# Optimization experiments

Measured on AMD Instinct MI355X. Metric: run time of the kernel, lower is better.

Reference implementation:

```python
import jax, jax.numpy as jnp
import numpy as np

B, CIN, MID, OUT = 4096, 64, 256, 256
K = CIN * 25  # flattened 5x5 patch per channel
EPS = 1e-5


def _masks():
    # [3, 25] binary masks over the 5x5 kernel for the 3 branch families
    circle = np.zeros((5, 5), np.float32); circle[1:4, 1:4] = 1.0
    corner = np.zeros((5, 5), np.float32)
    for (i, j) in [(0, 0), (0, 4), (4, 0), (4, 4), (2, 2)]:
        corner[i, j] = 1.0
    horse = np.zeros((5, 5), np.float32)
    for (i, j) in [(0, 1), (0, 3), (1, 0), (1, 4), (3, 0), (3, 4), (4, 1), (4, 3), (2, 2)]:
        horse[i, j] = 1.0
    return jnp.asarray(np.stack([circle, corner, horse]).reshape(3, 25))


def mish(x):
    return x * jnp.tanh(jax.nn.softplus(x))


def setup_inputs() -> dict:
    key = jax.random.key(0)
    ks = jax.random.split(key, 12)
    x = jax.random.normal(ks[0], (B, CIN, 7, 7), jnp.float32)
    W5 = jax.random.normal(ks[1], (27, MID, K), jnp.float32) * 0.05
    b5 = jax.random.normal(ks[2], (27, MID), jnp.float32) * 0.05
    gamma = jnp.ones((27, MID), jnp.float32)
    beta = jnp.zeros((27, MID), jnp.float32)
    run_mean = jax.random.normal(ks[3], (27, MID), jnp.float32) * 0.05
    run_var = jax.random.uniform(ks[4], (27, MID), jnp.float32, 0.5, 1.5)
    W1 = jax.random.normal(ks[5], (27, MID, MID), jnp.float32) * 0.05
    b1 = jax.random.normal(ks[6], (27, MID), jnp.float32) * 0.05
    W2 = jax.random.normal(ks[7], (27, OUT, MID), jnp.float32) * 0.05
    b2 = jax.random.normal(ks[8], (27, OUT), jnp.float32) * 0.05
    return {"x": x, "W5": W5, "b5": b5, "gamma": gamma, "beta": beta,
            "run_mean": run_mean, "run_var": run_var,
            "W1": W1, "b1": b1, "W2": W2, "b2": b2}


def reference(x, W5, b5, gamma, beta, run_mean, run_var, W1, b1, W2, b2):
    masks = _masks()  # [3,25]
    # 9 patches of 5x5: [9, B, CIN*25]
    patches = jnp.stack([x[:, :, k:k + 5, v:v + 5]
                         for k in range(3) for v in range(3)])
    patches = patches.reshape(9, B, K)
    # mask kernels per branch family and group weights as [3,9,MID,K]
    mask_k = jnp.repeat(masks, 9, axis=0)          # [27,25]
    mask_k = jnp.tile(mask_k, (1, CIN))[:, None, :]  # [27,1,CIN*25]
    W5m = (W5 * mask_k).reshape(3, 9, MID, K)
    # masked 5x5 conv on 5x5 patch -> 1x1 == dot product: [3,9,B,MID]
    z = jnp.einsum('pbk,gpmk->gpbm', patches, W5m) + b5.reshape(3, 9, 1, MID)
    # BatchNorm (inference, running stats) + Mish
    inv = jax.lax.rsqrt(run_var.reshape(3, 9, 1, MID) + EPS)
    h = mish((z - run_mean.reshape(3, 9, 1, MID)) * inv
             * gamma.reshape(3, 9, 1, MID) + beta.reshape(3, 9, 1, MID))
    # 1x1 conv + Mish, then final 1x1 conv
    h = mish(jnp.einsum('gpbm,gpnm->gpbn', h, W1.reshape(3, 9, MID, MID))
             + b1.reshape(3, 9, 1, MID))
    o = jnp.einsum('gpbm,gpom->gpbo', h, W2.reshape(3, 9, OUT, MID)) \
        + b2.reshape(3, 9, 1, OUT)                 # [3,9,B,OUT]
    copy_features = o[0].sum(0)                    # sum of 9 circle branches
    jump_features = o[1].sum(0) + o[2].sum(0)      # sum of 18 corner+horse
    # output is 1x1 spatially, so flatten(2).sum(2) is identity on [B,OUT]
    return copy_features * jump_features
```

## Files before the change

### kernel.cpp

```cpp
#include <hip/hip_runtime.h>

typedef __bf16 bf16x8 __attribute__((ext_vector_type(8)));
typedef float f32x4 __attribute__((ext_vector_type(4)));

__constant__ int SL_I[3][9] = {{1,1,1,2,2,2,3,3,3},{0,0,2,4,4,0,0,0,0},{0,0,1,1,2,3,3,4,4}};
__constant__ int SL_J[3][9] = {{1,2,3,1,2,3,1,2,3},{0,4,2,0,4,0,0,0,0},{1,3,0,4,2,0,4,1,3}};
__constant__ int SL_S[3][9] = {{6,7,8,11,12,13,16,17,18},{0,4,12,20,24,0,0,0,0},{1,3,5,9,12,15,19,21,23}};

#define GLDS16(gsrc, ldst)                                                        \
  __builtin_amdgcn_global_load_lds(                                               \
      (const __attribute__((address_space(1))) unsigned int*)(gsrc),              \
      (__attribute__((address_space(3))) unsigned int*)(ldst), 16, 0, 0)

static __device__ __forceinline__ unsigned short f2b(float f) {
  return __builtin_bit_cast(unsigned short, (__bf16)f);
}
static __device__ __forceinline__ float b2f(unsigned short u) {
  unsigned int b = ((unsigned int)u) << 16;
  return __builtin_bit_cast(float, b);
}
static __device__ __forceinline__ float mish_f(float x) {
  float u = __expf(x);
  float w = u * (u + 2.0f);
  float r = x * w * __builtin_amdgcn_rcpf(w + 2.0f);
  return (x > 20.0f) ? x : r;
}
static __device__ __forceinline__ int swz8(int c, int r) {
  return ((((c >> 3) ^ (r & 7)) << 3) | (c & 7));
}
static __device__ __forceinline__ int swoff(int c, int r) {
  return (c & ~63) | ((c & 63) ^ ((r & 7) << 3));
}

__global__ __launch_bounds__(256) void prep_x_k(const float* __restrict__ X,
                                                unsigned short* __restrict__ Xb) {
  __shared__ float tile[3136];
  const int b = blockIdx.x;
  const float* xp = X + (size_t)b * 3136;
  for (int i = threadIdx.x; i < 3136; i += 256) tile[i] = xp[i];
  __syncthreads();
  for (int i = threadIdx.x; i < 3136; i += 256) {
    int s = i >> 6, c = i & 63;
    Xb[(size_t)s * 262144 + (size_t)b * 64 + swz8(c, b)] = f2b(tile[c * 49 + s]);
  }
}

__global__ __launch_bounds__(256) void prep_w5_k(const float* __restrict__ W5,
                                                 unsigned short* __restrict__ W5c) {
  int idx = blockIdx.x * 256 + threadIdx.x;
  if (idx >= 27 * 256 * 9 * 64) return;
  int c = idx & 63;
  int t2 = idx >> 6;
  int u = t2 % 9;
  int gm = t2 / 9;
  int m = gm & 255;
  int g = (gm >> 8) / 9;
  int nm = (g == 1) ? 5 : 9;
  if (u >= nm) return;
  int c_src = swz8(c, m);
  W5c[idx] = f2b(W5[(size_t)gm * 1600 + c_src * 25 + SL_S[g][u]]);
}

__global__ __launch_bounds__(256) void prep_w12_k(const float* __restrict__ W1, const float* __restrict__ W2,
                                                  unsigned short* __restrict__ W1b, unsigned short* __restrict__ W2b) {
  int idx = blockIdx.x * 256 + threadIdx.x;
  if (idx < 27 * 256 * 256) {
    int n = (idx >> 8) & 255;
    int c = idx & 63;
    int src = (idx & ~63) | swz8(c, n);
    W1b[idx] = f2b(W1[src]);
    W2b[idx] = f2b(W2[src]);
  }
}

__global__ __launch_bounds__(256) void prep_bn_k(const float* __restrict__ b5, const float* __restrict__ gamma,
                                                 const float* __restrict__ beta, const float* __restrict__ rmean,
                                                 const float* __restrict__ rvar,
                                                 float* __restrict__ bn_a, float* __restrict__ bn_c) {
  int i = blockIdx.x * 256 + threadIdx.x;
  if (i < 27 * 256) {
    float a = gamma[i] * rsqrtf(rvar[i] + 1e-5f);
    bn_a[i] = a;
    bn_c[i] = (b5[i] - rmean[i]) * a + beta[i];
  }
}

__global__ __launch_bounds__(512) void gemm1_k(const unsigned short* __restrict__ Xb,
                                               const unsigned short* __restrict__ W5c,
                                               const float* __restrict__ bn_a, const float* __restrict__ bn_c,
                                               unsigned short* __restrict__ H) {
  __shared__ unsigned short smem[32768];
  const int t = threadIdx.x;
  const int lane = t & 63;
  const int w = t >> 6;
  const int wm = w >> 2, wn = w & 3;
  const int l15 = lane & 15, l4 = lane >> 4;
  const int sw = l15 & 7;
  const int m0 = blockIdx.x * 128, n0 = blockIdx.y * 128;
  const int gp = blockIdx.z;
  const int g = gp / 9, p = gp - g * 9;
  const int pk = p / 3, pv = p - pk * 3;
  const int nm = (g == 1) ? 5 : 9;

  const f32x4 zero = {0.f, 0.f, 0.f, 0.f};
  f32x4 acc[4][2];
#pragma unroll
  for (int i = 0; i < 4; ++i)
#pragma unroll
    for (int j = 0; j < 2; ++j) acc[i][j] = zero;

  auto STAGE = [&](int pbuf, int u) {
    const int s = (pk + SL_I[g][u]) * 7 + (pv + SL_J[g][u]);
    const unsigned short* srcA = Xb + (size_t)s * 262144 + (size_t)m0 * 64;
    unsigned short* dA = smem + pbuf * 16384;
    unsigned short* dB = dA + 8192;
#pragma unroll
    for (int it = 0; it < 2; ++it) {
      int idx = it * 512 + t;
      GLDS16(srcA + idx * 8, dA + idx * 8);
    }
#pragma unroll
    for (int it = 0; it < 2; ++it) {
      int idx = it * 512 + t;
      int row = idx >> 3, ch = idx & 7;
      GLDS16(W5c + (size_t)(gp * 256 + n0 + row) * 576 + u * 64 + ch * 8, dB + idx * 8);
    }
  };

  STAGE(0, 0);
  __syncthreads();
  int cur = 0;
  for (int u = 0; u < nm; ++u) {
    if (u + 1 < nm) STAGE(cur ^ 1, u + 1);
    const unsigned short* lA = smem + cur * 16384;
    const unsigned short* lB = lA + 8192;
#pragma unroll
    for (int kk = 0; kk < 2; ++kk) {
      bf16x8 af[4], bfr[2];
#pragma unroll
      for (int f4 = 0; f4 < 4; ++f4)
        af[f4] = *reinterpret_cast<const bf16x8*>(lA + (wm * 64 + f4 * 16 + l15) * 64 + (((kk * 4 + l4) ^ sw) << 3));
#pragma unroll
      for (int f2 = 0; f2 < 2; ++f2)
        bfr[f2] = *reinterpret_cast<const bf16x8*>(lB + (wn * 32 + f2 * 16 + l15) * 64 + (((kk * 4 + l4) ^ sw) << 3));
#pragma unroll
      for (int i = 0; i < 4; ++i)
#pragma unroll
        for (int j = 0; j < 2; ++j)
          acc[i][j] = __builtin_amdgcn_mfma_f32_16x16x32_bf16(af[i], bfr[j], acc[i][j], 0, 0, 0);
    }
    __syncthreads();
    cur ^= 1;
  }
#pragma unroll
  for (int j = 0; j < 2; ++j) {
    const int col = wn * 32 + j * 16 + l15;
    const float a  = bn_a[gp * 256 + n0 + col];
    const float cc = bn_c[gp * 256 + n0 + col];
#pragma unroll
    for (int i = 0; i < 4; ++i) {
      const int r0 = wm * 64 + i * 16 + l4 * 4;
#pragma unroll
      for (int e = 0; e < 4; ++e) {
        const int r = r0 + e;
        float z = acc[i][j][e] * a + cc;
        smem[r * 128 + (col ^ ((r & 7) << 3))] = f2b(mish_f(z));
      }
    }
  }
  __syncthreads();
  {
    unsigned short* Hg = H + (size_t)gp * 1048576;
#pragma unroll
    for (int it = 0; it < 4; ++it) {
      int idx = it * 512 + t;
      int row = idx >> 4, seg = idx & 15;
      int c8 = (seg * 8) ^ ((row & 7) << 3);
      uint4 v = *(const uint4*)(smem + row * 128 + c8);
      int colout = n0 + (seg >> 3) * 64 + (((seg & 7) ^ (row & 7)) << 3);
      *(uint4*)(Hg + (size_t)(m0 + row) * 256 + colout) = v;
    }
  }
}

__global__ __launch_bounds__(512) void gemm23f_k(const unsigned short* __restrict__ Hb,
                                                 const unsigned short* __restrict__ W1b,
                                                 const unsigned short* __restrict__ W2b,
                                                 const float* __restrict__ b1, const float* __restrict__ b2,
                                                 unsigned short* __restrict__ Obuf) {
  extern __shared__ unsigned short smem[];
  unsigned short* h1  = smem;
  unsigned short* stA = smem + 16384;
  unsigned short* stB = smem + 24576;
  const int t = threadIdx.x;
  const int lane = t & 63;
  const int w = t >> 6;
  const int wm = w >> 2, wn = w & 3;
  const int l15 = lane & 15, l4 = lane >> 4;
  const int sw = l15 & 7;
  const int m0 = blockIdx.x * 64;
  const int gp = blockIdx.y;

  const f32x4 zero = {0.f, 0.f, 0.f, 0.f};
  f32x4 acc[2][4];
#pragma unroll
  for (int i = 0; i < 2; ++i)
#pragma unroll
    for (int j = 0; j < 4; ++j) acc[i][j] = zero;

  auto STAGE_A = [&](int pbuf, int kt) {
    unsigned short* dA = stA + pbuf * 4096;
    GLDS16(Hb + (size_t)(gp * 4096 + m0 + (t >> 3)) * 256 + kt * 64 + (t & 7) * 8, dA + t * 8);
  };
  auto STAGE_B = [&](const unsigned short* W, int kt) {
#pragma unroll
    for (int it = 0; it < 4; ++it) {
      int idx = it * 512 + t;
      GLDS16(W + (size_t)(gp * 256 + (idx >> 3)) * 256 + kt * 64 + (idx & 7) * 8, stB + idx * 8);
    }
  };

  STAGE_A(0, 0);
  STAGE_B(W1b, 0);
  __syncthreads();
  int cur = 0;
  for (int kt = 0; kt < 4; ++kt) {
    if (kt < 3) STAGE_A(cur ^ 1, kt + 1);
    const unsigned short* lA = stA + cur * 4096;
#pragma unroll
    for (int kk = 0; kk < 2; ++kk) {
      bf16x8 af[2], bfr[4];
#pragma unroll
      for (int f2 = 0; f2 < 2; ++f2)
        af[f2] = *reinterpret_cast<const bf16x8*>(lA + (wm * 32 + f2 * 16 + l15) * 64 + (((kk * 4 + l4) ^ sw) << 3));
#pragma unroll
      for (int f4 = 0; f4 < 4; ++f4)
        bfr[f4] = *reinterpret_cast<const bf16x8*>(stB + (wn * 64 + f4 * 16 + l15) * 64 + (((kk * 4 + l4) ^ sw) << 3));
#pragma unroll
      for (int i = 0; i < 2; ++i)
#pragma unroll
        for (int j = 0; j < 4; ++j)
          acc[i][j] = __builtin_amdgcn_mfma_f32_16x16x32_bf16(af[i], bfr[j], acc[i][j], 0, 0, 0);
    }
    __syncthreads();
    if (kt < 3) {
      STAGE_B(W1b, kt + 1);
      __syncthreads();
    }
    cur ^= 1;
  }
#pragma unroll
  for (int j = 0; j < 4; ++j) {
    const int c = wn * 64 + j * 16 + l15;
    const float bi = b1[gp * 256 + c];
#pragma unroll
    for (int i = 0; i < 2; ++i) {
      const int r0 = wm * 32 + i * 16 + l4 * 4;
#pragma unroll
      for (int e = 0; e < 4; ++e) {
        const int r = r0 + e;
        h1[r * 256 + swoff(c, r)] = f2b(mish_f(acc[i][j][e] + bi));
      }
    }
  }
  __syncthreads();

#pragma unroll
  for (int i = 0; i < 2; ++i)
#pragma unroll
    for (int j = 0; j < 4; ++j) acc[i][j] = zero;
  for (int kt = 0; kt < 4; ++kt) {
    STAGE_B(W2b, kt);
    __syncthreads();
#pragma unroll
    for (int kk = 0; kk < 2; ++kk) {
      bf16x8 af[2], bfr[4];
#pragma unroll
      for (int f2 = 0; f2 < 2; ++f2)
        af[f2] = *reinterpret_cast<const bf16x8*>(
            h1 + (wm * 32 + f2 * 16 + l15) * 256 + kt * 64 + (((kk * 4 + l4) ^ sw) << 3));
#pragma unroll
      for (int f4 = 0; f4 < 4; ++f4)
        bfr[f4] = *reinterpret_cast<const bf16x8*>(stB + (wn * 64 + f4 * 16 + l15) * 64 + (((kk * 4 + l4) ^ sw) << 3));
#pragma unroll
      for (int i = 0; i < 2; ++i)
#pragma unroll
        for (int j = 0; j < 4; ++j)
          acc[i][j] = __builtin_amdgcn_mfma_f32_16x16x32_bf16(af[i], bfr[j], acc[i][j], 0, 0, 0);
    }
    __syncthreads();
  }
  unsigned short* tr = stA;
#pragma unroll
  for (int j = 0; j < 4; ++j) {
    const int c = wn * 64 + j * 16 + l15;
    const float bi = b2[gp * 256 + c];
#pragma unroll
    for (int i = 0; i < 2; ++i) {
      const int r0 = wm * 32 + i * 16 + l4 * 4;
#pragma unroll
      for (int e = 0; e < 4; ++e) {
        const int r = r0 + e;
        tr[r * 256 + swoff(c, r)] = f2b(acc[i][j][e] + bi);
      }
    }
  }
  __syncthreads();
  {
    unsigned short* Og = Obuf + (size_t)gp * 1048576;
#pragma unroll
    for (int it = 0; it < 4; ++it) {
      int idx = it * 512 + t;
      int row = idx >> 5, seg = idx & 31;
      int c8 = swoff(seg * 8, row);
      uint4 v = *(const uint4*)(tr + row * 256 + c8);
      *(uint4*)(Og + (size_t)(m0 + row) * 256 + seg * 8) = v;
    }
  }
}

__global__ __launch_bounds__(256) void final_k(const unsigned short* __restrict__ O, float* __restrict__ out) {
  const size_t base = ((size_t)blockIdx.x * 256 + threadIdx.x) * 8;
  float cs[8], js[8];
#pragma unroll
  for (int e = 0; e < 8; ++e) { cs[e] = 0.f; js[e] = 0.f; }
#pragma unroll
  for (int gp = 0; gp < 27; ++gp) {
    uint4 v = *(const uint4*)(O + (size_t)gp * 1048576 + base);
    const unsigned short* pv = (const unsigned short*)&v;
    if (gp < 9) {
#pragma unroll
      for (int e = 0; e < 8; ++e) cs[e] += b2f(pv[e]);
    } else {
#pragma unroll
      for (int e = 0; e < 8; ++e) js[e] += b2f(pv[e]);
    }
  }
  float4 o0 = {cs[0] * js[0], cs[1] * js[1], cs[2] * js[2], cs[3] * js[3]};
  float4 o1 = {cs[4] * js[4], cs[5] * js[5], cs[6] * js[6], cs[7] * js[7]};
  *(float4*)(out + base) = o0;
  *(float4*)(out + base + 4) = o1;
}

extern "C" void kernel_launch(void* const* d_in, const int* in_sizes, int n_in,
                              void* d_out, int out_size, void* d_ws, size_t ws_size,
                              hipStream_t stream) {
  const float* X     = (const float*)d_in[0];
  const float* W5    = (const float*)d_in[1];
  const float* b5    = (const float*)d_in[2];
  const float* gamma = (const float*)d_in[3];
  const float* beta  = (const float*)d_in[4];
  const float* rmean = (const float*)d_in[5];
  const float* rvar  = (const float*)d_in[6];
  const float* W1    = (const float*)d_in[7];
  const float* b1    = (const float*)d_in[8];
  const float* W2    = (const float*)d_in[9];
  const float* b2    = (const float*)d_in[10];
  float* out = (float*)d_out;
  char* ws = (char*)d_ws;

  unsigned short* W5c  = (unsigned short*)(ws);
  unsigned short* W1b  = (unsigned short*)(ws + 7962624);
  unsigned short* W2b  = (unsigned short*)(ws + 11501568);
  float*          bn_a = (float*)(ws + 15040512);
  float*          bn_c = (float*)(ws + 15068160);
  unsigned short* Xb   = (unsigned short*)(ws + 15095808);
  unsigned short* Hbuf = (unsigned short*)(ws + 40785920);
  unsigned short* Obuf = (unsigned short*)(ws + 97409024);

  (void)hipFuncSetAttribute(reinterpret_cast<const void*>(gemm23f_k),
                            hipFuncAttributeMaxDynamicSharedMemorySize, 81920);

  prep_x_k<<<4096, 256, 0, stream>>>(X, Xb);
  prep_w5_k<<<15552, 256, 0, stream>>>(W5, W5c);
  prep_w12_k<<<6912, 256, 0, stream>>>(W1, W2, W1b, W2b);
  prep_bn_k<<<27, 256, 0, stream>>>(b5, gamma, beta, rmean, rvar, bn_a, bn_c);

  gemm1_k<<<dim3(32, 2, 27), 512, 0, stream>>>(Xb, W5c, bn_a, bn_c, Hbuf);
  gemm23f_k<<<dim3(64, 27), 512, 81920, stream>>>(Hbuf, W1b, W2b, b1, b2, Obuf);
  final_k<<<512, 256, 0, stream>>>(Obuf, out);
}
```

Before: 161.6 us.

## Pre-tile weights into MFMA fragment order and double-buffer B staging

The weight prep kernels now write W5, W1 and W2 in a k-chunk-major, fragment-ready tiled layout, with each thread converting and storing 8 values with vector stores. The GEMM kernels then load B tiles as contiguous blocks and read fragments without the XOR swizzle. In gemm23f the B tile is now double-buffered with K=32 steps, so the next weight tile is prefetched during compute. This removes an extra barrier per step and the strided row loads. The cost is more loop iterations and barriers at finer granularity, plus a changed LDS read pattern that may bring bank conflicts.

```diff
diff --git a/kernel.cpp b/kernel.cpp
--- a/kernel.cpp
+++ b/kernel.cpp
@@ -47,30 +47,54 @@
 
 __global__ __launch_bounds__(256) void prep_w5_k(const float* __restrict__ W5,
                                                  unsigned short* __restrict__ W5c) {
-  int idx = blockIdx.x * 256 + threadIdx.x;
-  if (idx >= 27 * 256 * 9 * 64) return;
-  int c = idx & 63;
-  int t2 = idx >> 6;
-  int u = t2 % 9;
-  int gm = t2 / 9;
-  int m = gm & 255;
-  int g = (gm >> 8) / 9;
+  int tid = blockIdx.x * 256 + threadIdx.x;
+  if (tid >= 497664) return;
+  int n  = tid & 127;
+  int r1 = tid >> 7;
+  int q  = r1 & 7;
+  int r2 = r1 >> 3;
+  int nt = r2 & 1;
+  int r3 = r2 >> 1;
+  int u  = r3 % 9;
+  int gp = r3 / 9;
+  int g = gp / 9;
   int nm = (g == 1) ? 5 : 9;
   if (u >= nm) return;
-  int c_src = swz8(c, m);
-  W5c[idx] = f2b(W5[(size_t)gm * 1600 + c_src * 25 + SL_S[g][u]]);
+  int s = SL_S[g][u];
+  const float* src = W5 + (size_t)(gp * 256 + nt * 128 + n) * 1600 + s;
+  unsigned short* dst = W5c + (size_t)tid * 8;
+  ushort4 v0, v1;
+  float a0 = src[(q * 8 + 0) * 25], a1 = src[(q * 8 + 1) * 25];
+  float a2 = src[(q * 8 + 2) * 25], a3 = src[(q * 8 + 3) * 25];
+  float a4 = src[(q * 8 + 4) * 25], a5 = src[(q * 8 + 5) * 25];
+  float a6 = src[(q * 8 + 6) * 25], a7 = src[(q * 8 + 7) * 25];
+  v0 = {f2b(a0), f2b(a1), f2b(a2), f2b(a3)};
+  v1 = {f2b(a4), f2b(a5), f2b(a6), f2b(a7)};
+  *(ushort4*)(dst) = v0;
+  *(ushort4*)(dst + 4) = v1;
 }
 
 __global__ __launch_bounds__(256) void prep_w12_k(const float* __restrict__ W1, const float* __restrict__ W2,
-                                                  unsigned short* __restrict__ W1b, unsigned short* __restrict__ W2b) {
-  int idx = blockIdx.x * 256 + threadIdx.x;
-  if (idx < 27 * 256 * 256) {
-    int n = (idx >> 8) & 255;
-    int c = idx & 63;
-    int src = (idx & ~63) | swz8(c, n);
-    W1b[idx] = f2b(W1[src]);
-    W2b[idx] = f2b(W2[src]);
-  }
+                                                  unsigned short* __restrict__ W1c, unsigned short* __restrict__ W2c) {
+  int tid = blockIdx.x * 256 + threadIdx.x;
+  if (tid >= 221184) return;
+  int n  = tid & 255;
+  int q  = (tid >> 8) & 3;
+  int kt = (tid >> 10) & 7;
+  int gp = tid >> 13;
+  size_t src = (size_t)(gp * 256 + n) * 256 + kt * 32 + q * 8;
+  float4 a0 = *(const float4*)(W1 + src);
+  float4 a1 = *(const float4*)(W1 + src + 4);
+  float4 b0 = *(const float4*)(W2 + src);
+  float4 b1 = *(const float4*)(W2 + src + 4);
+  ushort4 ua0 = {f2b(a0.x), f2b(a0.y), f2b(a0.z), f2b(a0.w)};
+  ushort4 ua1 = {f2b(a1.x), f2b(a1.y), f2b(a1.z), f2b(a1.w)};
+  ushort4 ub0 = {f2b(b0.x), f2b(b0.y), f2b(b0.z), f2b(b0.w)};
+  ushort4 ub1 = {f2b(b1.x), f2b(b1.y), f2b(b1.z), f2b(b1.w)};
+  *(ushort4*)(W1c + (size_t)tid * 8) = ua0;
+  *(ushort4*)(W1c + (size_t)tid * 8 + 4) = ua1;
+  *(ushort4*)(W2c + (size_t)tid * 8) = ub0;
+  *(ushort4*)(W2c + (size_t)tid * 8 + 4) = ub1;
 }
 
 __global__ __launch_bounds__(256) void prep_bn_k(const float* __restrict__ b5, const float* __restrict__ gamma,
@@ -97,6 +121,7 @@
   const int l15 = lane & 15, l4 = lane >> 4;
   const int sw = l15 & 7;
   const int m0 = blockIdx.x * 128, n0 = blockIdx.y * 128;
+  const int nt = blockIdx.y;
   const int gp = blockIdx.z;
   const int g = gp / 9, p = gp - g * 9;
   const int pk = p / 3, pv = p - pk * 3;
@@ -112,6 +137,7 @@
   auto STAGE = [&](int pbuf, int u) {
     const int s = (pk + SL_I[g][u]) * 7 + (pv + SL_J[g][u]);
     const unsigned short* srcA = Xb + (size_t)s * 262144 + (size_t)m0 * 64;
+    const unsigned short* srcB = W5c + ((size_t)((gp * 9 + u) * 2 + nt)) * 8192;
     unsigned short* dA = smem + pbuf * 16384;
     unsigned short* dB = dA + 8192;
 #pragma unroll
@@ -122,8 +148,7 @@
 #pragma unroll
     for (int it = 0; it < 2; ++it) {
       int idx = it * 512 + t;
-      int row = idx >> 3, ch = idx & 7;
-      GLDS16(W5c + (size_t)(gp * 256 + n0 + row) * 576 + u * 64 + ch * 8, dB + idx * 8);
+      GLDS16(srcB + idx * 8, dB + idx * 8);
     }
   };
 
@@ -142,7 +167,7 @@
         af[f4] = *reinterpret_cast<const bf16x8*>(lA + (wm * 64 + f4 * 16 + l15) * 64 + (((kk * 4 + l4) ^ sw) << 3));
 #pragma unroll
       for (int f2 = 0; f2 < 2; ++f2)
-        bfr[f2] = *reinterpret_cast<const bf16x8*>(lB + (wn * 32 + f2 * 16 + l15) * 64 + (((kk * 4 + l4) ^ sw) << 3));
+        bfr[f2] = *reinterpret_cast<const bf16x8*>(lB + (kk * 4 + l4) * 1024 + (wn * 32 + f2 * 16 + l15) * 8);
 #pragma unroll
       for (int i = 0; i < 4; ++i)
 #pragma unroll
@@ -184,8 +209,8 @@
 }
 
 __global__ __launch_bounds__(512) void gemm23f_k(const unsigned short* __restrict__ Hb,
-                                                 const unsigned short* __restrict__ W1b,
-                                                 const unsigned short* __restrict__ W2b,
+                                                 const unsigned short* __restrict__ W1c,
+                                                 const unsigned short* __restrict__ W2c,
                                                  const float* __restrict__ b1, const float* __restrict__ b2,
                                                  unsigned short* __restrict__ Obuf) {
   extern __shared__ unsigned short smem[];
@@ -208,47 +233,46 @@
 #pragma unroll
     for (int j = 0; j < 4; ++j) acc[i][j] = zero;
 
-  auto STAGE_A = [&](int pbuf, int kt) {
+  auto STAGE_A = [&](int pbuf, int kt64) {
     unsigned short* dA = stA + pbuf * 4096;
-    GLDS16(Hb + (size_t)(gp * 4096 + m0 + (t >> 3)) * 256 + kt * 64 + (t & 7) * 8, dA + t * 8);
+    GLDS16(Hb + (size_t)(gp * 4096 + m0 + (t >> 3)) * 256 + kt64 * 64 + (t & 7) * 8, dA + t * 8);
   };
-  auto STAGE_B = [&](const unsigned short* W, int kt) {
-#pragma unroll
-    for (int it = 0; it < 4; ++it) {
+  auto STAGE_B = [&](const unsigned short* Wc, int kt32, int pbuf) {
+    unsigned short* dB = stB + pbuf * 8192;
+    const unsigned short* src = Wc + ((size_t)(gp * 8 + kt32)) * 8192;
+#pragma unroll
+    for (int it = 0; it < 2; ++it) {
       int idx = it * 512 + t;
-      GLDS16(W + (size_t)(gp * 256 + (idx >> 3)) * 256 + kt * 64 + (idx & 7) * 8, stB + idx * 8);
+      GLDS16(src + idx * 8, dB + idx * 8);
     }
   };
 
   STAGE_A(0, 0);
-  STAGE_B(W1b, 0);
-  __syncthreads();
-  int cur = 0;
-  for (int kt = 0; kt < 4; ++kt) {
-    if (kt < 3) STAGE_A(cur ^ 1, kt + 1);
-    const unsigned short* lA = stA + cur * 4096;
-#pragma unroll
-    for (int kk = 0; kk < 2; ++kk) {
-      bf16x8 af[2], bfr[4];
-#pragma unroll
-      for (int f2 = 0; f2 < 2; ++f2)
-        af[f2] = *reinterpret_cast<const bf16x8*>(lA + (wm * 32 + f2 * 16 + l15) * 64 + (((kk * 4 + l4) ^ sw) << 3));
-#pragma unroll
-      for (int f4 = 0; f4 < 4; ++f4)
-        bfr[f4] = *reinterpret_cast<const bf16x8*>(stB + (wn * 64 + f4 * 16 + l15) * 64 + (((kk * 4 + l4) ^ sw) << 3));
-#pragma unroll
-      for (int i = 0; i < 2; ++i)
-#pragma unroll
-        for (int j = 0; j < 4; ++j)
-          acc[i][j] = __builtin_amdgcn_mfma_f32_16x16x32_bf16(af[i], bfr[j], acc[i][j], 0, 0, 0);
-    }
+  STAGE_B(W1c, 0, 0);
+  __syncthreads();
+  int curA = 0, curB = 0;
+  for (int kt = 0; kt < 8; ++kt) {
+    if (kt + 1 < 8) STAGE_B(W1c, kt + 1, curB ^ 1);
+    if ((kt & 1) == 0 && kt + 2 < 8) STAGE_A(curA ^ 1, (kt >> 1) + 1);
+    const unsigned short* lA = stA + curA * 4096;
+    const unsigned short* lB = stB + curB * 8192;
+    bf16x8 af[2], bfr[4];
+#pragma unroll
+    for (int f2 = 0; f2 < 2; ++f2)
+      af[f2] = *reinterpret_cast<const bf16x8*>(lA + (wm * 32 + f2 * 16 + l15) * 64 + ((((kt & 1) * 4 + l4) ^ sw) << 3));
+#pragma unroll
+    for (int f4 = 0; f4 < 4; ++f4)
+      bfr[f4] = *reinterpret_cast<const bf16x8*>(lB + l4 * 2048 + (wn * 64 + f4 * 16 + l15) * 8);
+#pragma unroll
+    for (int i = 0; i < 2; ++i)
+#pragma unroll
+      for (int j = 0; j < 4; ++j)
+        acc[i][j] = __builtin_amdgcn_mfma_f32_16x16x32_bf16(af[i], bfr[j], acc[i][j], 0, 0, 0);
     __syncthreads();
-    if (kt < 3) {
-      STAGE_B(W1b, kt + 1);
-      __syncthreads();
-    }
-    cur ^= 1;
-  }
+    curB ^= 1;
+    if (kt & 1) curA ^= 1;
+  }
+  STAGE_B(W2c, 0, 0);
 #pragma unroll
   for (int j = 0; j < 4; ++j) {
     const int c = wn * 64 + j * 16 + l15;
@@ -269,26 +293,27 @@
   for (int i = 0; i < 2; ++i)
 #pragma unroll
     for (int j = 0; j < 4; ++j) acc[i][j] = zero;
-  for (int kt = 0; kt < 4; ++kt) {
-    STAGE_B(W2b, kt);
+  curB = 0;
+  for (int kt = 0; kt < 8; ++kt) {
+    if (kt + 1 < 8) STAGE_B(W2c, kt + 1, curB ^ 1);
+    const unsigned short* lB = stB + curB * 8192;
+    bf16x8 af[2], bfr[4];
+#pragma unroll
+    for (int f2 = 0; f2 < 2; ++f2) {
+      const int row = wm * 32 + f2 * 16 + l15;
+      af[f2] = *reinterpret_cast<const bf16x8*>(
+          h1 + row * 256 + (kt >> 1) * 64 + ((((kt & 1) * 4 + l4) ^ sw) << 3));
+    }
+#pragma unroll
+    for (int f4 = 0; f4 < 4; ++f4)
+      bfr[f4] = *reinterpret_cast<const bf16x8*>(lB + l4 * 2048 + (wn * 64 + f4 * 16 + l15) * 8);
+#pragma unroll
+    for (int i = 0; i < 2; ++i)
+#pragma unroll
+      for (int j = 0; j < 4; ++j)
+        acc[i][j] = __builtin_amdgcn_mfma_f32_16x16x32_bf16(af[i], bfr[j], acc[i][j], 0, 0, 0);
     __syncthreads();
-#pragma unroll
-    for (int kk = 0; kk < 2; ++kk) {
-      bf16x8 af[2], bfr[4];
-#pragma unroll
-      for (int f2 = 0; f2 < 2; ++f2)
-        af[f2] = *reinterpret_cast<const bf16x8*>(
-            h1 + (wm * 32 + f2 * 16 + l15) * 256 + kt * 64 + (((kk * 4 + l4) ^ sw) << 3));
-#pragma unroll
-      for (int f4 = 0; f4 < 4; ++f4)
-        bfr[f4] = *reinterpret_cast<const bf16x8*>(stB + (wn * 64 + f4 * 16 + l15) * 64 + (((kk * 4 + l4) ^ sw) << 3));
-#pragma unroll
-      for (int i = 0; i < 2; ++i)
-#pragma unroll
-        for (int j = 0; j < 4; ++j)
-          acc[i][j] = __builtin_amdgcn_mfma_f32_16x16x32_bf16(af[i], bfr[j], acc[i][j], 0, 0, 0);
-    }
-    __syncthreads();
+    curB ^= 1;
   }
   unsigned short* tr = stA;
 #pragma unroll
@@ -360,8 +385,8 @@
   char* ws = (char*)d_ws;
 
   unsigned short* W5c  = (unsigned short*)(ws);
-  unsigned short* W1b  = (unsigned short*)(ws + 7962624);
-  unsigned short* W2b  = (unsigned short*)(ws + 11501568);
+  unsigned short* W1c  = (unsigned short*)(ws + 7962624);
+  unsigned short* W2c  = (unsigned short*)(ws + 11501568);
   float*          bn_a = (float*)(ws + 15040512);
   float*          bn_c = (float*)(ws + 15068160);
   unsigned short* Xb   = (unsigned short*)(ws + 15095808);
@@ -372,11 +397,11 @@
                             hipFuncAttributeMaxDynamicSharedMemorySize, 81920);
 
   prep_x_k<<<4096, 256, 0, stream>>>(X, Xb);
-  prep_w5_k<<<15552, 256, 0, stream>>>(W5, W5c);
-  prep_w12_k<<<6912, 256, 0, stream>>>(W1, W2, W1b, W2b);
+  prep_w5_k<<<1944, 256, 0, stream>>>(W5, W5c);
+  prep_w12_k<<<864, 256, 0, stream>>>(W1, W2, W1c, W2c);
   prep_bn_k<<<27, 256, 0, stream>>>(b5, gamma, beta, rmean, rvar, bn_a, bn_c);
 
   gemm1_k<<<dim3(32, 2, 27), 512, 0, stream>>>(Xb, W5c, bn_a, bn_c, Hbuf);
-  gemm23f_k<<<dim3(64, 27), 512, 81920, stream>>>(Hbuf, W1b, W2b, b1, b2, Obuf);
+  gemm23f_k<<<dim3(64, 27), 512, 81920, stream>>>(Hbuf, W1c, W2c, b1, b2, Obuf);
   final_k<<<512, 256, 0, stream>>>(Obuf, out);
 }
```

Measured after the change: 161.8 us. No clear change (+0.1%).
